# Performance work log

Hardware: AMD Instinct MI355X
Metric: run time of the kernel (lower is better)

## Reference

```python
import jax, jax.numpy as jnp
import numpy as np

IGNORE_ID = -1
NEG_INF = -jnp.inf


def ctc_force_align(log_probs, ctc_label):
    """Viterbi forced alignment, vectorized over batch, scan over time.

    log_probs: [B, T, V] log-softmaxed CTC outputs (blank = 0).
    ctc_label: [B, L] int labels in [1, V).
    Returns align: [B, L] float32, begin frame (1-based, t+1) of each label.
    Assumes uniform lengths: input_len = T, target_len = L for every item
    (how the inputs are generated here).
    """
    B, T, V = log_probs.shape
    L = ctc_label.shape[1]
    N = 2 * L + 1  # CTC state lattice: blank,label,blank,...

    labels = jnp.zeros((B, N), dtype=ctc_label.dtype).at[:, 1::2].set(ctc_label)
    # per-state emission log-prob: [B, T, N]
    lab_b = jnp.broadcast_to(labels[:, None, :], (B, T, N))
    lp_states = jnp.take_along_axis(log_probs, lab_b, axis=2)

    idx = jnp.arange(N)
    ihalf = idx.astype(jnp.float32) / 2.0
    # labels[i] == labels[i-2] (False for i < 2)
    same_label = labels == jnp.concatenate(
        [jnp.full((B, 2), -1, labels.dtype), labels[:, :-2]], axis=1)
    two_way = (idx % 2 == 0)[None, :] | (idx == 1)[None, :] | same_label  # [B, N]

    ts = jnp.arange(T).astype(jnp.float32)
    # infeasible if i/2 > t or L - i/2 > T - t  (float division as in original)
    feas = ~((ihalf[None, :] > ts[:, None]) |
             (float(L) - ihalf[None, :] > float(T) - ts[:, None]))  # [T, N]

    a0 = jnp.where(idx[None, :] < 2, lp_states[:, 0, :], NEG_INF)  # [B, N]

    def shift(x, k):
        return jnp.pad(x, ((0, 0), (k, 0)), constant_values=NEG_INF)[:, :N]

    def step(a_prev, inputs):
        lp_t, feas_t = inputs  # [B, N], [N]
        p0, p1, p2 = a_prev, shift(a_prev, 1), shift(a_prev, 2)
        val_two = jnp.where(p0 > p1, idx, idx - 1)
        best0 = (p0 > p1) & (p0 > p2)
        best1 = (p1 > p0) & (p1 > p2)
        val_three = jnp.where(best0, idx, jnp.where(best1, idx - 1, idx - 2))
        val = jnp.where(idx[None, :] == 0, 0,
                        jnp.where(two_way, val_two, val_three))
        off = idx[None, :] - val
        a_sel = jnp.where(off == 0, p0, jnp.where(off == 1, p1, p2))
        a_new = jnp.where(feas_t[None, :], a_sel + lp_t, NEG_INF)
        v = jnp.where(feas_t[None, :], val, 0).astype(jnp.int32)
        return a_new, v

    lp_tb = jnp.moveaxis(lp_states, 1, 0)  # [T, B, N]
    a_final, v_all = jax.lax.scan(step, a0, (lp_tb[1:], feas[1:]))
    # v_all: [T-1, B, N] for t = 1 .. T-1
    v_all = jnp.moveaxis(v_all, 1, 0)  # [B, T-1, N]

    def backtrace(a_fin, v_seq):  # a_fin: [N], v_seq: [T-1, N]
        use_last = a_fin[N - 1] > a_fin[N - 2]
        pre0 = jnp.where(use_last, N - 1, N - 2)
        align0 = jnp.where((jnp.arange(L) == L - 1) & (~use_last),
                           float(T), 0.0).astype(jnp.float32)
        tp1 = jnp.arange(T - 1, 0, -1)  # t+1 values: T-1 .. 1
        lidx = jnp.arange(L)

        def bstep(carry, inp):
            pre, align = carry
            v_row, t1 = inp
            pre = v_row[pre]
            odd = (pre % 2) == 1
            align = jnp.where((lidx == pre // 2) & odd,
                              t1.astype(jnp.float32), align)
            return (pre, align), None

        (_, align), _ = jax.lax.scan(bstep, (pre0, align0), (v_seq[::-1], tp1))
        return align

    return jax.vmap(backtrace)(a_final, v_all)  # [B, L]


def setup_inputs() -> dict:
    key = jax.random.key(0)
    k0, k1, k2, k3, k4 = jax.random.split(key, 5)
    B, layers, L, T, V = 16, 6, 200, 1000, 5000
    ali_out = jax.random.uniform(k0, (B, layers, L + 1, T), dtype=jnp.float32)
    ali_beg = jax.random.randint(k1, (B, L), 0, T, dtype=jnp.int32)
    ali_end = jax.random.randint(k2, (B, L), 0, T, dtype=jnp.int32)
    enc_mask = jnp.zeros((B, T), dtype=bool)
    ctc_out = jax.random.normal(k3, (B, T, V), dtype=jnp.float32)
    ctc_label = jax.random.randint(k4, (B, L), 1, V, dtype=jnp.int32)
    ctc_len = jnp.full((B,), T, dtype=jnp.int32)
    return {"ali_out": ali_out, "ali_beg": ali_beg, "ali_end": ali_end,
            "enc_mask": enc_mask, "ctc_out": ctc_out,
            "ctc_label": ctc_label, "ctc_len": ctc_len}


def reference(ali_out, ali_beg, ali_end, enc_mask, ctc_out, ctc_label, ctc_len):
    B, layers, olen, ilen = ali_out.shape
    hlen = enc_mask.shape[1]  # == ilen == T
    # forced alignment on detached (stop-gradient) log-probs
    log_probs = jax.lax.stop_gradient(jax.nn.log_softmax(ctc_out, axis=2))
    ali = ctc_force_align(log_probs, ctc_label)  # [B, L] float32
    # expected position: matmul with pos_vec = [1..hlen], drop last output step
    pos = jnp.arange(1, hlen + 1, dtype=ali_out.dtype)
    ali_pos = jnp.einsum('bloi,i->blo', ali_out, pos)[:, :, :-1]  # [B, layers, L]
    ylens = jnp.sum(ali_beg != IGNORE_ID, axis=1)  # [B]
    mask = jnp.arange(olen - 1)[None, :] >= ylens[:, None]  # [B, L] pad mask
    total = (~mask).sum().astype(ali_out.dtype) * layers
    lat = jnp.where(mask[:, None, :], 0.0, ali_pos - ali[:, None, :])
    return (lat ** 2).sum() / total / hlen
```

## Files before the change

### kernel.cpp

```cpp
#include <hip/hip_runtime.h>
#include <hip/hip_bf16.h>
#include <math.h>

#define NEGINF (-INFINITY)

typedef float f32x4 __attribute__((ext_vector_type(4)));

__device__ __forceinline__ float wave_max_f(float m) {
#pragma unroll
  for (int d = 32; d > 0; d >>= 1) m = fmaxf(m, __shfl_xor(m, d, 64));
  return m;
}
__device__ __forceinline__ float wave_sum_f(float s) {
#pragma unroll
  for (int d = 32; d > 0; d >>= 1) s += __shfl_xor(s, d, 64);
  return s;
}
__device__ __forceinline__ int wave_sum_i(int s) {
#pragma unroll
  for (int d = 32; d > 0; d >>= 1) s += __shfl_xor(s, d, 64);
  return s;
}

__device__ __forceinline__ float dpp_wave_shr1(float x) {
  int r = __builtin_amdgcn_mov_dpp(__float_as_int(x), 0x138, 0xf, 0xf, true);
  return __int_as_float(r);
}

__global__ __launch_bounds__(256) void kA_lse_gather(
    const float* __restrict__ ctc_out, const int* __restrict__ ctc_label,
    float* __restrict__ lp, int B, int T, int V, int L, int LANES,
    int TPAD, int ROWF)
{
  extern __shared__ float shrow[];
  __shared__ float wred[4];
  int row = blockIdx.x;
  int b = row / T;
  int t = row - b * T;
  int tid = threadIdx.x;
  int w = tid >> 6;
  const float* x = ctc_out + (size_t)row * V;

  float m = NEGINF;
  int nf4 = V >> 2;
  for (int k = tid; k < nf4; k += 256) {
    float4 v = reinterpret_cast<const float4*>(x)[k];
    reinterpret_cast<float4*>(shrow)[k] = v;
    m = fmaxf(m, fmaxf(fmaxf(v.x, v.y), fmaxf(v.z, v.w)));
  }
  for (int k = (nf4 << 2) + tid; k < V; k += 256) {
    float v = x[k]; shrow[k] = v; m = fmaxf(m, v);
  }
  m = wave_max_f(m);
  if ((tid & 63) == 0) wred[w] = m;
  __syncthreads();
  float bm = fmaxf(fmaxf(wred[0], wred[1]), fmaxf(wred[2], wred[3]));
  __syncthreads();

  float s = 0.f;
  for (int k = tid; k < V; k += 256) s += __expf(shrow[k] - bm);
  s = wave_sum_f(s);
  if ((tid & 63) == 0) wred[w] = s;
  __syncthreads();
  float lse = bm + __logf(wred[0] + wred[1] + wred[2] + wred[3]);

  const int* lab = ctc_label + (size_t)b * L;
  float* dst = lp + ((size_t)b * TPAD + t) * ROWF;
  int nq = LANES * 4;
  for (int idx = tid; idx < nq; idx += 256) {
    int sl = idx >> 2, q = idx & 3;
    int jb = ((7 * sl) >> 1) + 1;
    int j = jb + q; if (j > L) j = L;
    int vi = lab[j - 1];
    if ((unsigned)vi >= (unsigned)V) vi = 0;
    dst[idx] = shrow[vi] - lse;
  }
  if (tid == 0) dst[nq] = shrow[0] - lse;
}

__global__ __launch_bounds__(64, 1) void kB_viterbi(
    const float* __restrict__ lp, const int* __restrict__ ctc_label,
    float* __restrict__ ali, int B, int T, int L, int TPAD, int ROWF)
{
  extern __shared__ float smemf[];
  const int N = 2 * L + 1;
  const int LANES = (N + 6) / 7;
  const unsigned STGB = (unsigned)(16 * ROWF * 4);
  const unsigned OFFROW = 2u * STGB;

  int b = blockIdx.x;
  int lane = threadIdx.x;
  const float* lpb = lp + (size_t)b * TPAD * ROWF;
  const int* lab = ctc_label + (size_t)b * L;
  int qlane = (lane < LANES) ? lane : (LANES - 1);
  int blkoff = LANES * 4;
  unsigned sbase = __builtin_amdgcn_groupstaticsize();

  int i0 = lane * 7;
  float a0v, a1v, a2v, a3v, a4v, a5v, a6v;
  int twv[7];
  int tlo[7];
  unsigned rng[7];
#pragma unroll
  for (int s = 0; s < 7; ++s) {
    int i = i0 + s;
    bool valid = (i < N);
    bool odd = (i & 1) != 0;
    int li = (i - 1) >> 1;
    int myl = (odd && valid) ? lab[li] : 0;
    int pl  = (odd && valid && i >= 3) ? lab[li - 1] : -1;
    twv[s] = ((!odd) || (i == 1) || (myl == pl)) ? 1 : 0;
    if (valid) {
      tlo[s] = (i + 1) >> 1;
      int thi = T - L + (i >> 1);
      rng[s] = (unsigned)(thi - tlo[s]);
    } else {
      tlo[s] = T + 2;
      rng[s] = 0u;
    }
  }

  {
    f32x4 q00 = reinterpret_cast<const f32x4*>(lpb)[qlane];
    float bl00 = lpb[blkoff];
    a0v = (i0 == 0) ? bl00 : NEGINF;
    a1v = NEGINF; a2v = NEGINF; a3v = NEGINF; a4v = NEGINF; a5v = NEGINF;
    a6v = NEGINF;
    if (i0 + 1 == 1) a1v = q00.x;
  }

  int ndma = ROWF >> 4;
#define DMA_SEG(row0, bufidx)                                                 \
  {                                                                           \
    const float* gsrc_ = lpb + (size_t)(row0) * ROWF;                         \
    char* dbase_ = (char*)smemf + (unsigned)(bufidx) * STGB;                  \
    for (int kk_ = 0; kk_ < ndma; ++kk_) {                                    \
      __builtin_amdgcn_global_load_lds(                                       \
          (const unsigned int*)(gsrc_ + (size_t)kk_ * 256 + lane * 4),        \
          (unsigned int*)(dbase_ + kk_ * 1024), 16, 0, 0);                    \
    }                                                                         \
  }

  f32x4 rqA, rqB, rqC, rqD;
  float rblA, rblB, rblC, rblD;

#define RINGRD(SL, qaddr, baddr)                                              \
  asm volatile("ds_read_b128 %0, %1" : "=v"(rq##SL) : "v"(qaddr));            \
  asm volatile("ds_read_b32 %0, %1" : "=v"(rbl##SL) : "v"(baddr));

#define STEP_F(s, P0, P1, P2, OCS, ND, OD)                                    \
  {                                                                           \
    bool c01 = (P0) > (P1);                                                   \
    float m01 = c01 ? (P0) : (P1);                                            \
    bool take3 = (twv[s] == 0) && !(m01 > (P2));                              \
    float asel = take3 ? (P2) : m01;                                          \
    OD = take3 ? 2u : (c01 ? 0u : 1u);                                        \
    float lps = (((lane + (s)) & 1) ? (OCS) : blc);                           \
    ND = asel + lps;                                                          \
  }

#define STEP_S(s, P0, P1, P2, OCS, ND, OD)                                    \
  {                                                                           \
    STEP_F(s, P0, P1, P2, OCS, ND, OD)                                        \
    bool feas = (unsigned)(tt - tlo[s]) <= rng[s];                            \
    ND = feas ? ND : NEGINF;                                                  \
  }

#define BODY(SL, UL, STEPM)                                                   \
  {                                                                           \
    const int tt = tt0 + (UL);                                                \
    asm volatile("s_waitcnt lgkmcnt(9)");                                     \
    __builtin_amdgcn_sched_barrier(0);                                        \
    float blc = rbl##SL;                                                      \
    f32x4 oc = rq##SL;                                                        \
    float n0, n1, n2, n3, n4, n5, n6;                                         \
    unsigned o0, o1, o2, o3, o4, o5, o6;                                      \
    STEPM(5, a5v, a4v, a3v, oc.z, n5, o5)                                     \
    STEPM(6, a6v, a5v, a4v, oc.w, n6, o6)                                     \
    float t6n = dpp_wave_shr1(n6);                                            \
    float t5n = dpp_wave_shr1(n5);                                            \
    STEPM(0, a0v, t6, t5, oc.x, n0, o0)                                       \
    STEPM(1, a1v, a0v, t6, oc.x, n1, o1)                                      \
    STEPM(2, a2v, a1v, a0v, oc.y, n2, o2)                                     \
    STEPM(3, a3v, a2v, a1v, oc.y, n3, o3)                                     \
    STEPM(4, a4v, a3v, a2v, oc.z, n4, o4)                                     \
    unsigned pack = o0 | (o1 << 2) | (o2 << 4) | (o3 << 6) | (o4 << 8) |      \
                    (o5 << 10) | (o6 << 12);                                  \
    asm volatile("ds_write_b16 %0, %1" :: "v"(wa), "v"(pack));                \
    wa += 128;                                                                \
    if ((UL) == 12) {                                                         \
      asm volatile("s_waitcnt vmcnt(0)" ::: "memory");                        \
      __builtin_amdgcn_sched_barrier(0);                                      \
    }                                                                         \
    {                                                                         \
      unsigned qa = ((UL) < 12) ? (qcur + ((UL) + 4) * 960u)                  \
                                : (qnxt + ((UL) - 12) * 960u);                \
      unsigned ba = ((UL) < 12) ? (bcur + ((UL) + 4) * 960u)                  \
                                : (bnxt + ((UL) - 12) * 960u);                \
      RINGRD(SL, qa, ba)                                                      \
    }                                                                         \
    a0v = n0; a1v = n1; a2v = n2; a3v = n3; a4v = n4; a5v = n5; a6v = n6;     \
    t6 = (lane == 0) ? NEGINF : t6n;                                          \
    t5 = (lane == 0) ? NEGINF : t5n;                                          \
  }

  DMA_SEG(1, 0)
  asm volatile("s_waitcnt vmcnt(0)" ::: "memory");
  __builtin_amdgcn_sched_barrier(0);

  unsigned wa = sbase + OFFROW + (unsigned)(lane * 2);
  {
    unsigned q0 = sbase + (unsigned)(qlane * 16);
    unsigned b0 = sbase + (unsigned)(blkoff * 4);
    RINGRD(A, q0 + 0u * 960u, b0 + 0u * 960u)
    RINGRD(B, q0 + 1u * 960u, b0 + 1u * 960u)
    RINGRD(C, q0 + 2u * 960u, b0 + 2u * 960u)
    RINGRD(D, q0 + 3u * 960u, b0 + 3u * 960u)
    unsigned zz = 0;
    asm volatile("ds_write_b16 %0, %1" :: "v"(wa), "v"(zz));
    asm volatile("ds_write_b16 %0, %1" :: "v"(wa), "v"(zz));
    asm volatile("ds_write_b16 %0, %1" :: "v"(wa), "v"(zz));
  }

  float t6 = __shfl_up(a6v, 1, 64);
  float t5 = __shfl_up(a5v, 1, 64);
  if (lane == 0) { t6 = NEGINF; t5 = NEGINF; }

  int NSEG = (T - 1 + 15) >> 4;
  for (int sg = 0; sg < NSEG; ++sg) {
    int tt0 = 1 + 16 * sg;
    unsigned bufc = sbase + (unsigned)(sg & 1) * STGB;
    unsigned bufn = sbase + (unsigned)((sg + 1) & 1) * STGB;
    unsigned qcur = bufc + (unsigned)(qlane * 16);
    unsigned qnxt = bufn + (unsigned)(qlane * 16);
    unsigned bcur = bufc + (unsigned)(blkoff * 4);
    unsigned bnxt = bufn + (unsigned)(blkoff * 4);
    if (sg + 1 < NSEG) { DMA_SEG(tt0 + 16, ((sg + 1) & 1)) }
    int rem = T - tt0;
    bool fast = (rem >= 16) && (tt0 >= L) && (tt0 + 15 <= T - L);
    if (fast) {
      BODY(A, 0, STEP_F)  BODY(B, 1, STEP_F)  BODY(C, 2, STEP_F)
      BODY(D, 3, STEP_F)  BODY(A, 4, STEP_F)  BODY(B, 5, STEP_F)
      BODY(C, 6, STEP_F)  BODY(D, 7, STEP_F)  BODY(A, 8, STEP_F)
      BODY(B, 9, STEP_F)  BODY(C, 10, STEP_F) BODY(D, 11, STEP_F)
      BODY(A, 12, STEP_F) BODY(B, 13, STEP_F) BODY(C, 14, STEP_F)
      BODY(D, 15, STEP_F)
    } else {
      if (0 < rem)  { BODY(A, 0, STEP_S) }
      if (1 < rem)  { BODY(B, 1, STEP_S) }
      if (2 < rem)  { BODY(C, 2, STEP_S) }
      if (3 < rem)  { BODY(D, 3, STEP_S) }
      if (4 < rem)  { BODY(A, 4, STEP_S) }
      if (5 < rem)  { BODY(B, 5, STEP_S) }
      if (6 < rem)  { BODY(C, 6, STEP_S) }
      if (7 < rem)  { BODY(D, 7, STEP_S) }
      if (8 < rem)  { BODY(A, 8, STEP_S) }
      if (9 < rem)  { BODY(B, 9, STEP_S) }
      if (10 < rem) { BODY(C, 10, STEP_S) }
      if (11 < rem) { BODY(D, 11, STEP_S) }
      if (12 < rem) { BODY(A, 12, STEP_S) }
      if (13 < rem) { BODY(B, 13, STEP_S) }
      if (14 < rem) { BODY(C, 14, STEP_S) }
      if (15 < rem) { BODY(D, 15, STEP_S) }
    }
  }
#undef BODY
#undef STEP_S
#undef STEP_F
#undef RINGRD
#undef DMA_SEG

  asm volatile("s_waitcnt vmcnt(0) lgkmcnt(0)" ::: "memory");
  __builtin_amdgcn_sched_barrier(0);

  int iN1 = N - 1, iN2 = N - 2;
  auto pick = [&](int sIdx) {
    float r = a0v;
    r = (sIdx == 1) ? a1v : r;
    r = (sIdx == 2) ? a2v : r;
    r = (sIdx == 3) ? a3v : r;
    r = (sIdx == 4) ? a4v : r;
    r = (sIdx == 5) ? a5v : r;
    r = (sIdx == 6) ? a6v : r;
    return r;
  };
  float vlast = __shfl(pick(iN1 % 7), iN1 / 7, 64);
  float vprev = __shfl(pick(iN2 % 7), iN2 / 7, 64);
  bool use_last = vlast > vprev;
  int pre = use_last ? iN1 : iN2;

  float al[4] = {0.f, 0.f, 0.f, 0.f};
  {
    int lbl = L - 1; int rr = lbl >> 6, ln = lbl & 63;
#pragma unroll
    for (int r = 0; r < 4; ++r)
      if (!use_last && rr == r && lane == ln) al[r] = (float)T;
  }

  const unsigned short* offrow =
      (const unsigned short*)((char*)smemf + OFFROW);
  int t = T - 1;
  int g = pre / 7, mm = pre - g * 7;
  while (t >= 1) {
    int K = (t < 7) ? t : 7;
    int pcur = g * 7 + mm;
    int gmax = g;
    unsigned short w0v = offrow[(size_t)(t - 1) * 64 + g];
    unsigned short cw[7][3];
    int gmn[7];
#pragma unroll
    for (int j = 1; j < 7; ++j) {
      if (j < K) {
        int lo = pcur - 2 * j; if (lo < 0) lo = 0;
        int gm = lo / 7;
        gmn[j] = gm;
#pragma unroll
        for (int r = 0; r < 3; ++r) {
          int gg = gm + r; if (gg > gmax) gg = gmax;
          cw[j][r] = offrow[(size_t)(t - 1 - j) * 64 + gg];
        }
      }
    }
#pragma unroll
    for (int j = 0; j < 7; ++j) {
      if (j < K) {
        unsigned w;
        if (j == 0) {
          w = w0v;
        } else {
          int gi = g - gmn[j];
          unsigned wva = cw[j][0], wvb = cw[j][1], wvc = cw[j][2];
          w = (gi == 0) ? wva : ((gi == 1) ? wvb : wvc);
        }
        unsigned off = (w >> (2 * mm)) & 3u;
        mm -= (int)off;
        bool bor = mm < 0;
        g = bor ? (g - 1) : g;
        mm = bor ? (mm + 7) : mm;
        int cur = g * 7 + mm;
        if (cur & 1) {
          int lbl = cur >> 1;
          int rr = lbl >> 6, ln = lbl & 63;
#pragma unroll
          for (int r = 0; r < 4; ++r)
            if (rr == r && lane == ln) al[r] = (float)(t - j);
        }
      }
    }
    t -= K;
  }

#pragma unroll
  for (int r = 0; r < 4; ++r) {
    int l = lane + 64 * r;
    if (l < L) ali[(size_t)b * L + l] = al[r];
  }
}

__global__ __launch_bounds__(256) void kC_rows(
    const float* __restrict__ ali_out, const float* __restrict__ ali,
    const int* __restrict__ ali_beg, float* __restrict__ partials,
    int B, int layers, int L, int T)
{
  __shared__ float ps[4];
  int wid = threadIdx.x >> 6, lane = threadIdx.x & 63;
  int row = blockIdx.x * 4 + wid;
  int nrows = B * layers * L;
  float val = 0.f;
  if (row < nrows) {
    int o = row % L;
    int bl = row / L;
    int layer = bl % layers;
    int b = bl / layers;
    const float* x = ali_out + ((size_t)(b * layers + layer) * (L + 1) + o) * T;
    float s = 0.f;
    if ((T & 3) == 0) {
      int nf4 = T >> 2;
      for (int k = lane; k < nf4; k += 64) {
        float4 v = reinterpret_cast<const float4*>(x)[k];
        float base = (float)(4 * k);
        s += v.x * (base + 1.f) + v.y * (base + 2.f) +
             v.z * (base + 3.f) + v.w * (base + 4.f);
      }
    } else {
      for (int k = lane; k < T; k += 64) s += x[k] * (float)(k + 1);
    }
    s = wave_sum_f(s);
    int cnt = 0;
    for (int l = lane; l < L; l += 64)
      cnt += (ali_beg[(size_t)b * L + l] != -1) ? 1 : 0;
    cnt = wave_sum_i(cnt);
    if (lane == 0) {
      float lat = (o >= cnt) ? 0.f : (s - ali[(size_t)b * L + o]);
      val = lat * lat;
    }
  }
  if (lane == 0) ps[wid] = val;
  __syncthreads();
  if (threadIdx.x == 0) partials[blockIdx.x] = ps[0] + ps[1] + ps[2] + ps[3];
}

__global__ __launch_bounds__(256) void kD_final(
    const float* __restrict__ partials, int nparts,
    const int* __restrict__ ali_beg, int BL, int layers, int T,
    float* __restrict__ out)
{
  __shared__ float wred[4];
  __shared__ int wcnt[4];
  int tid = threadIdx.x, w = tid >> 6;
  float s = 0.f;
  for (int k = tid; k < nparts; k += 256) s += partials[k];
  s = wave_sum_f(s);
  int c = 0;
  for (int k = tid; k < BL; k += 256) c += (ali_beg[k] != -1) ? 1 : 0;
  c = wave_sum_i(c);
  if ((tid & 63) == 0) { wred[w] = s; wcnt[w] = c; }
  __syncthreads();
  if (tid == 0) {
    float ss = wred[0] + wred[1] + wred[2] + wred[3];
    float total = (float)(wcnt[0] + wcnt[1] + wcnt[2] + wcnt[3]) * (float)layers;
    out[0] = ss / total / (float)T;
  }
}

extern "C" void kernel_launch(void* const* d_in, const int* in_sizes, int n_in,
                              void* d_out, int out_size, void* d_ws, size_t ws_size,
                              hipStream_t stream)
{
  const float* ali_out   = (const float*)d_in[0];
  const int*   ali_beg   = (const int*)d_in[1];
  const float* ctc_out   = (const float*)d_in[4];
  const int*   ctc_label = (const int*)d_in[5];

  int B = in_sizes[6];
  int L = in_sizes[1] / B;
  int T = in_sizes[3] / B;
  int V = (int)((long long)in_sizes[4] / ((long long)B * T));
  int layers = (int)((long long)in_sizes[0] / ((long long)B * (L + 1) * T));

  int N = 2 * L + 1;
  int LANES = (N + 6) / 7;
  int ROWF = LANES * 4 + 8;
  int TPAD = T + 64;

  float* lp = (float*)d_ws;
  float* ali = lp + (size_t)B * TPAD * ROWF;
  float* partials = ali + (size_t)B * L;
  int nrows = B * layers * L;
  int gridC = (nrows + 3) / 4;

  size_t shA = (size_t)V * sizeof(float);
  hipLaunchKernelGGL(kA_lse_gather, dim3(B * T), dim3(256), shA, stream,
                     ctc_out, ctc_label, lp, B, T, V, L, LANES, TPAD, ROWF);

  size_t shB = (size_t)2 * 16 * ROWF * sizeof(float) + (size_t)(T - 1) * 128;
  hipFuncSetAttribute(reinterpret_cast<const void*>(kB_viterbi),
                      hipFuncAttributeMaxDynamicSharedMemorySize, (int)shB);
  hipLaunchKernelGGL(kB_viterbi, dim3(B), dim3(64), shB, stream,
                     lp, ctc_label, ali, B, T, L, TPAD, ROWF);

  hipLaunchKernelGGL(kC_rows, dim3(gridC), dim3(256), 0, stream,
                     ali_out, ali, ali_beg, partials, B, layers, L, T);

  hipLaunchKernelGGL(kD_final, dim3(1), dim3(256), 0, stream,
                     partials, gridC, ali_beg, B * L, layers, T, (float*)d_out);
}
```

Baseline: 498.9 us.

## Deepen LDS read ring to eight slots and restructure DMA/wait schedule

Expands the register ring of prefetched LDS reads from four to eight slots, so each step's emission data is requested eight steps ahead. The next segment's global-to-LDS DMA now starts inside the first step of each segment, with full waits at steps 0 and 8 in place of a per-step lgkmcnt(9) wait. The feasibility-free fast path is removed, so every full segment applies the feasibility mask. The trade-off is more VGPRs, extra feasibility work on every step, and coarser full-drain waits that may stall the serial recurrence.

```diff
diff --git a/kernel.cpp b/kernel.cpp
--- a/kernel.cpp
+++ b/kernel.cpp
@@ -139,16 +139,17 @@
           (const unsigned int*)(gsrc_ + (size_t)kk_ * 256 + lane * 4),        \
           (unsigned int*)(dbase_ + kk_ * 1024), 16, 0, 0);                    \
     }                                                                         \
-  }
-
-  f32x4 rqA, rqB, rqC, rqD;
-  float rblA, rblB, rblC, rblD;
+    __builtin_amdgcn_sched_barrier(0);                                        \
+  }
+
+  f32x4 rqA, rqB, rqC, rqD, rqE, rqF, rqG, rqH;
+  float rblA, rblB, rblC, rblD, rblE, rblF, rblG, rblH;
 
 #define RINGRD(SL, qaddr, baddr)                                              \
   asm volatile("ds_read_b128 %0, %1" : "=v"(rq##SL) : "v"(qaddr));            \
   asm volatile("ds_read_b32 %0, %1" : "=v"(rbl##SL) : "v"(baddr));
 
-#define STEP_F(s, P0, P1, P2, OCS, ND, OD)                                    \
+#define STEP(s, P0, P1, P2, OCS, ND, OD)                                      \
   {                                                                           \
     bool c01 = (P0) > (P1);                                                   \
     float m01 = c01 ? (P0) : (P1);                                            \
@@ -157,46 +158,78 @@
     OD = take3 ? 2u : (c01 ? 0u : 1u);                                        \
     float lps = (((lane + (s)) & 1) ? (OCS) : blc);                           \
     ND = asel + lps;                                                          \
-  }
-
-#define STEP_S(s, P0, P1, P2, OCS, ND, OD)                                    \
-  {                                                                           \
-    STEP_F(s, P0, P1, P2, OCS, ND, OD)                                        \
     bool feas = (unsigned)(tt - tlo[s]) <= rng[s];                            \
     ND = feas ? ND : NEGINF;                                                  \
   }
 
-#define BODY(SL, UL, STEPM)                                                   \
+#define BODY(SL, UL)                                                          \
   {                                                                           \
     const int tt = tt0 + (UL);                                                \
-    asm volatile("s_waitcnt lgkmcnt(9)");                                     \
+    if ((UL) == 0) {                                                          \
+      asm volatile("s_waitcnt lgkmcnt(0)");                                   \
+      __builtin_amdgcn_sched_barrier(0);                                      \
+      if (sg + 1 < NSEG) { DMA_SEG(tt0 + 16, ((sg + 1) & 1)) }                \
+    }                                                                         \
+    if ((UL) == 8) {                                                          \
+      asm volatile("s_waitcnt vmcnt(0) lgkmcnt(0)");                          \
+      __builtin_amdgcn_sched_barrier(0);                                      \
+    }                                                                         \
+    float blc = rbl##SL;                                                      \
+    f32x4 oc = rq##SL;                                                        \
+    float n0, n1, n2, n3, n4, n5, n6;                                         \
+    unsigned o0, o1, o2, o3, o4, o5, o6;                                      \
+    STEP(5, a5v, a4v, a3v, oc.z, n5, o5)                                      \
+    STEP(6, a6v, a5v, a4v, oc.w, n6, o6)                                      \
+    float t6n = dpp_wave_shr1(n6);                                            \
+    float t5n = dpp_wave_shr1(n5);                                            \
+    STEP(0, a0v, t6, t5, oc.x, n0, o0)                                        \
+    STEP(1, a1v, a0v, t6, oc.x, n1, o1)                                       \
+    STEP(2, a2v, a1v, a0v, oc.y, n2, o2)                                      \
+    STEP(3, a3v, a2v, a1v, oc.y, n3, o3)                                      \
+    STEP(4, a4v, a3v, a2v, oc.z, n4, o4)                                      \
+    unsigned pack = o0 | (o1 << 2) | (o2 << 4) | (o3 << 6) | (o4 << 8) |      \
+                    (o5 << 10) | (o6 << 12);                                  \
+    asm volatile("ds_write_b16 %0, %1" :: "v"(wa), "v"(pack));                \
+    wa += 128;                                                                \
+    {                                                                         \
+      unsigned qa = ((UL) < 8) ? (qcur + ((UL) + 8) * 960u)                   \
+                               : (qnxt + ((UL) - 8) * 960u);                  \
+      unsigned ba = ((UL) < 8) ? (bcur + ((UL) + 8) * 960u)                   \
+                               : (bnxt + ((UL) - 8) * 960u);                  \
+      RINGRD(SL, qa, ba)                                                      \
+    }                                                                         \
+    a0v = n0; a1v = n1; a2v = n2; a3v = n3; a4v = n4; a5v = n5; a6v = n6;     \
+    t6 = (lane == 0) ? NEGINF : t6n;                                          \
+    t5 = (lane == 0) ? NEGINF : t5n;                                          \
+  }
+
+#define TBODY(SL, UL)                                                         \
+  {                                                                           \
+    const int tt = tt0 + (UL);                                                \
+    asm volatile("s_waitcnt vmcnt(0) lgkmcnt(0)");                            \
     __builtin_amdgcn_sched_barrier(0);                                        \
     float blc = rbl##SL;                                                      \
     f32x4 oc = rq##SL;                                                        \
     float n0, n1, n2, n3, n4, n5, n6;                                         \
     unsigned o0, o1, o2, o3, o4, o5, o6;                                      \
-    STEPM(5, a5v, a4v, a3v, oc.z, n5, o5)                                     \
-    STEPM(6, a6v, a5v, a4v, oc.w, n6, o6)                                     \
+    STEP(5, a5v, a4v, a3v, oc.z, n5, o5)                                      \
+    STEP(6, a6v, a5v, a4v, oc.w, n6, o6)                                      \
     float t6n = dpp_wave_shr1(n6);                                            \
     float t5n = dpp_wave_shr1(n5);                                            \
-    STEPM(0, a0v, t6, t5, oc.x, n0, o0)                                       \
-    STEPM(1, a1v, a0v, t6, oc.x, n1, o1)                                      \
-    STEPM(2, a2v, a1v, a0v, oc.y, n2, o2)                                     \
-    STEPM(3, a3v, a2v, a1v, oc.y, n3, o3)                                     \
-    STEPM(4, a4v, a3v, a2v, oc.z, n4, o4)                                     \
+    STEP(0, a0v, t6, t5, oc.x, n0, o0)                                        \
+    STEP(1, a1v, a0v, t6, oc.x, n1, o1)                                       \
+    STEP(2, a2v, a1v, a0v, oc.y, n2, o2)                                      \
+    STEP(3, a3v, a2v, a1v, oc.y, n3, o3)                                      \
+    STEP(4, a4v, a3v, a2v, oc.z, n4, o4)                                      \
     unsigned pack = o0 | (o1 << 2) | (o2 << 4) | (o3 << 6) | (o4 << 8) |      \
                     (o5 << 10) | (o6 << 12);                                  \
     asm volatile("ds_write_b16 %0, %1" :: "v"(wa), "v"(pack));                \
     wa += 128;                                                                \
-    if ((UL) == 12) {                                                         \
-      asm volatile("s_waitcnt vmcnt(0)" ::: "memory");                        \
-      __builtin_amdgcn_sched_barrier(0);                                      \
-    }                                                                         \
     {                                                                         \
-      unsigned qa = ((UL) < 12) ? (qcur + ((UL) + 4) * 960u)                  \
-                                : (qnxt + ((UL) - 12) * 960u);                \
-      unsigned ba = ((UL) < 12) ? (bcur + ((UL) + 4) * 960u)                  \
-                                : (bnxt + ((UL) - 12) * 960u);                \
+      unsigned qa = ((UL) < 8) ? (qcur + ((UL) + 8) * 960u)                   \
+                               : (qnxt + ((UL) - 8) * 960u);                  \
+      unsigned ba = ((UL) < 8) ? (bcur + ((UL) + 8) * 960u)                   \
+                               : (bnxt + ((UL) - 8) * 960u);                  \
       RINGRD(SL, qa, ba)                                                      \
     }                                                                         \
     a0v = n0; a1v = n1; a2v = n2; a3v = n3; a4v = n4; a5v = n5; a6v = n6;     \
@@ -205,7 +238,7 @@
   }
 
   DMA_SEG(1, 0)
-  asm volatile("s_waitcnt vmcnt(0)" ::: "memory");
+  asm volatile("s_waitcnt vmcnt(0) lgkmcnt(0)");
   __builtin_amdgcn_sched_barrier(0);
 
   unsigned wa = sbase + OFFROW + (unsigned)(lane * 2);
@@ -216,10 +249,10 @@
     RINGRD(B, q0 + 1u * 960u, b0 + 1u * 960u)
     RINGRD(C, q0 + 2u * 960u, b0 + 2u * 960u)
     RINGRD(D, q0 + 3u * 960u, b0 + 3u * 960u)
-    unsigned zz = 0;
-    asm volatile("ds_write_b16 %0, %1" :: "v"(wa), "v"(zz));
-    asm volatile("ds_write_b16 %0, %1" :: "v"(wa), "v"(zz));
-    asm volatile("ds_write_b16 %0, %1" :: "v"(wa), "v"(zz));
+    RINGRD(E, q0 + 4u * 960u, b0 + 4u * 960u)
+    RINGRD(F, q0 + 5u * 960u, b0 + 5u * 960u)
+    RINGRD(G, q0 + 6u * 960u, b0 + 6u * 960u)
+    RINGRD(H, q0 + 7u * 960u, b0 + 7u * 960u)
   }
 
   float t6 = __shfl_up(a6v, 1, 64);
@@ -235,38 +268,34 @@
     unsigned qnxt = bufn + (unsigned)(qlane * 16);
     unsigned bcur = bufc + (unsigned)(blkoff * 4);
     unsigned bnxt = bufn + (unsigned)(blkoff * 4);
-    if (sg + 1 < NSEG) { DMA_SEG(tt0 + 16, ((sg + 1) & 1)) }
     int rem = T - tt0;
-    bool fast = (rem >= 16) && (tt0 >= L) && (tt0 + 15 <= T - L);
-    if (fast) {
-      BODY(A, 0, STEP_F)  BODY(B, 1, STEP_F)  BODY(C, 2, STEP_F)
-      BODY(D, 3, STEP_F)  BODY(A, 4, STEP_F)  BODY(B, 5, STEP_F)
-      BODY(C, 6, STEP_F)  BODY(D, 7, STEP_F)  BODY(A, 8, STEP_F)
-      BODY(B, 9, STEP_F)  BODY(C, 10, STEP_F) BODY(D, 11, STEP_F)
-      BODY(A, 12, STEP_F) BODY(B, 13, STEP_F) BODY(C, 14, STEP_F)
-      BODY(D, 15, STEP_F)
+    if (rem >= 16) {
+      BODY(A, 0)  BODY(B, 1)  BODY(C, 2)  BODY(D, 3)
+      BODY(E, 4)  BODY(F, 5)  BODY(G, 6)  BODY(H, 7)
+      BODY(A, 8)  BODY(B, 9)  BODY(C, 10) BODY(D, 11)
+      BODY(E, 12) BODY(F, 13) BODY(G, 14) BODY(H, 15)
     } else {
-      if (0 < rem)  { BODY(A, 0, STEP_S) }
-      if (1 < rem)  { BODY(B, 1, STEP_S) }
-      if (2 < rem)  { BODY(C, 2, STEP_S) }
-      if (3 < rem)  { BODY(D, 3, STEP_S) }
-      if (4 < rem)  { BODY(A, 4, STEP_S) }
-      if (5 < rem)  { BODY(B, 5, STEP_S) }
-      if (6 < rem)  { BODY(C, 6, STEP_S) }
-      if (7 < rem)  { BODY(D, 7, STEP_S) }
-      if (8 < rem)  { BODY(A, 8, STEP_S) }
-      if (9 < rem)  { BODY(B, 9, STEP_S) }
-      if (10 < rem) { BODY(C, 10, STEP_S) }
-      if (11 < rem) { BODY(D, 11, STEP_S) }
-      if (12 < rem) { BODY(A, 12, STEP_S) }
-      if (13 < rem) { BODY(B, 13, STEP_S) }
-      if (14 < rem) { BODY(C, 14, STEP_S) }
-      if (15 < rem) { BODY(D, 15, STEP_S) }
-    }
-  }
+      if (0 < rem)  { TBODY(A, 0) }
+      if (1 < rem)  { TBODY(B, 1) }
+      if (2 < rem)  { TBODY(C, 2) }
+      if (3 < rem)  { TBODY(D, 3) }
+      if (4 < rem)  { TBODY(E, 4) }
+      if (5 < rem)  { TBODY(F, 5) }
+      if (6 < rem)  { TBODY(G, 6) }
+      if (7 < rem)  { TBODY(H, 7) }
+      if (8 < rem)  { TBODY(A, 8) }
+      if (9 < rem)  { TBODY(B, 9) }
+      if (10 < rem) { TBODY(C, 10) }
+      if (11 < rem) { TBODY(D, 11) }
+      if (12 < rem) { TBODY(E, 12) }
+      if (13 < rem) { TBODY(F, 13) }
+      if (14 < rem) { TBODY(G, 14) }
+      if (15 < rem) { TBODY(H, 15) }
+    }
+  }
+#undef TBODY
 #undef BODY
-#undef STEP_S
-#undef STEP_F
+#undef STEP
 #undef RINGRD
 #undef DMA_SEG
 
```

Measured after the change: 523.9 us. 5.0% more time.

## Replace LDS DMA ring with direct 8-deep register-prefetched global loads in Viterbi

Applied to the files above, without the earlier changes.

The Viterbi kernel stops staging emission rows through a double-buffered LDS ring filled by global_load_lds. Each lane now issues global_load_dwordx4 straight into an 8-entry register ring, and the blank emission is taken via readlane from lane 58 instead of a separate LDS read. The intent is to take the LDS round-trip and the per-segment DMA waits off the serial time recurrence and to shrink shared memory to just the backpointer table. In exchange, global load latency is exposed within an 8-step prefetch window. The padding columns are zeroed in kA so the extra lane can read defined data.

```diff
diff --git a/kernel.cpp b/kernel.cpp
--- a/kernel.cpp
+++ b/kernel.cpp
@@ -76,6 +76,7 @@
     dst[idx] = shrow[vi] - lse;
   }
   if (tid == 0) dst[nq] = shrow[0] - lse;
+  for (int z = nq + 1 + tid; z < ROWF; z += 256) dst[z] = 0.f;
 }
 
 __global__ __launch_bounds__(64, 1) void kB_viterbi(
@@ -85,16 +86,14 @@
   extern __shared__ float smemf[];
   const int N = 2 * L + 1;
   const int LANES = (N + 6) / 7;
-  const unsigned STGB = (unsigned)(16 * ROWF * 4);
-  const unsigned OFFROW = 2u * STGB;
 
   int b = blockIdx.x;
   int lane = threadIdx.x;
   const float* lpb = lp + (size_t)b * TPAD * ROWF;
   const int* lab = ctc_label + (size_t)b * L;
-  int qlane = (lane < LANES) ? lane : (LANES - 1);
+  int qlane = (lane < LANES) ? lane : LANES;
+  if (qlane > LANES) qlane = LANES;
   int blkoff = LANES * 4;
-  unsigned sbase = __builtin_amdgcn_groupstaticsize();
 
   int i0 = lane * 7;
   float a0v, a1v, a2v, a3v, a4v, a5v, a6v;
@@ -121,7 +120,7 @@
   }
 
   {
-    f32x4 q00 = reinterpret_cast<const f32x4*>(lpb)[qlane];
+    f32x4 q00 = *reinterpret_cast<const f32x4*>(lpb + qlane * 4);
     float bl00 = lpb[blkoff];
     a0v = (i0 == 0) ? bl00 : NEGINF;
     a1v = NEGINF; a2v = NEGINF; a3v = NEGINF; a4v = NEGINF; a5v = NEGINF;
@@ -129,24 +128,21 @@
     if (i0 + 1 == 1) a1v = q00.x;
   }
 
-  int ndma = ROWF >> 4;
-#define DMA_SEG(row0, bufidx)                                                 \
-  {                                                                           \
-    const float* gsrc_ = lpb + (size_t)(row0) * ROWF;                         \
-    char* dbase_ = (char*)smemf + (unsigned)(bufidx) * STGB;                  \
-    for (int kk_ = 0; kk_ < ndma; ++kk_) {                                    \
-      __builtin_amdgcn_global_load_lds(                                       \
-          (const unsigned int*)(gsrc_ + (size_t)kk_ * 256 + lane * 4),        \
-          (unsigned int*)(dbase_ + kk_ * 1024), 16, 0, 0);                    \
-    }                                                                         \
-  }
-
-  f32x4 rqA, rqB, rqC, rqD;
-  float rblA, rblB, rblC, rblD;
-
-#define RINGRD(SL, qaddr, baddr)                                              \
-  asm volatile("ds_read_b128 %0, %1" : "=v"(rq##SL) : "v"(qaddr));            \
-  asm volatile("ds_read_b32 %0, %1" : "=v"(rbl##SL) : "v"(baddr));
+  f32x4 rq0, rq1, rq2, rq3, rq4, rq5, rq6, rq7;
+  unsigned short* offrow_w = (unsigned short*)smemf;
+
+  asm volatile("s_waitcnt vmcnt(0) lgkmcnt(0)");
+  __builtin_amdgcn_sched_barrier(0);
+
+  unsigned long long base64 = (unsigned long long)lpb;
+  unsigned voff = (unsigned)(qlane * 16) + 960u;
+
+#define LOADQ(SL)                                                             \
+  asm volatile("global_load_dwordx4 %0, %1, %2"                               \
+               : "=v"(rq##SL) : "v"(voff), "s"(base64));                      \
+  voff += 960u;
+
+  LOADQ(1) LOADQ(2) LOADQ(3) LOADQ(4) LOADQ(5) LOADQ(6) LOADQ(7) LOADQ(0)
 
 #define STEP_F(s, P0, P1, P2, OCS, ND, OD)                                    \
   {                                                                           \
@@ -166,112 +162,68 @@
     ND = feas ? ND : NEGINF;                                                  \
   }
 
-#define BODY(SL, UL, STEPM)                                                   \
+#define BODYC(SL, K, STEPM)                                                   \
   {                                                                           \
-    const int tt = tt0 + (UL);                                                \
-    asm volatile("s_waitcnt lgkmcnt(9)");                                     \
+    const int tt = tt0 + (K);                                                 \
+    asm volatile("s_waitcnt vmcnt(7)");                                       \
     __builtin_amdgcn_sched_barrier(0);                                        \
-    float blc = rbl##SL;                                                      \
-    f32x4 oc = rq##SL;                                                        \
+    float blc = __int_as_float(                                               \
+        __builtin_amdgcn_readlane(__float_as_int(rq##SL.x), 58));             \
     float n0, n1, n2, n3, n4, n5, n6;                                         \
     unsigned o0, o1, o2, o3, o4, o5, o6;                                      \
-    STEPM(5, a5v, a4v, a3v, oc.z, n5, o5)                                     \
-    STEPM(6, a6v, a5v, a4v, oc.w, n6, o6)                                     \
+    STEPM(5, a5v, a4v, a3v, rq##SL.z, n5, o5)                                 \
+    STEPM(6, a6v, a5v, a4v, rq##SL.w, n6, o6)                                 \
     float t6n = dpp_wave_shr1(n6);                                            \
     float t5n = dpp_wave_shr1(n5);                                            \
-    STEPM(0, a0v, t6, t5, oc.x, n0, o0)                                       \
-    STEPM(1, a1v, a0v, t6, oc.x, n1, o1)                                      \
-    STEPM(2, a2v, a1v, a0v, oc.y, n2, o2)                                     \
-    STEPM(3, a3v, a2v, a1v, oc.y, n3, o3)                                     \
-    STEPM(4, a4v, a3v, a2v, oc.z, n4, o4)                                     \
+    STEPM(0, a0v, t6, t5, rq##SL.x, n0, o0)                                   \
+    STEPM(1, a1v, a0v, t6, rq##SL.x, n1, o1)                                  \
+    STEPM(2, a2v, a1v, a0v, rq##SL.y, n2, o2)                                 \
+    STEPM(3, a3v, a2v, a1v, rq##SL.y, n3, o3)                                 \
+    STEPM(4, a4v, a3v, a2v, rq##SL.z, n4, o4)                                 \
     unsigned pack = o0 | (o1 << 2) | (o2 << 4) | (o3 << 6) | (o4 << 8) |      \
                     (o5 << 10) | (o6 << 12);                                  \
-    asm volatile("ds_write_b16 %0, %1" :: "v"(wa), "v"(pack));                \
-    wa += 128;                                                                \
-    if ((UL) == 12) {                                                         \
-      asm volatile("s_waitcnt vmcnt(0)" ::: "memory");                        \
-      __builtin_amdgcn_sched_barrier(0);                                      \
-    }                                                                         \
-    {                                                                         \
-      unsigned qa = ((UL) < 12) ? (qcur + ((UL) + 4) * 960u)                  \
-                                : (qnxt + ((UL) - 12) * 960u);                \
-      unsigned ba = ((UL) < 12) ? (bcur + ((UL) + 4) * 960u)                  \
-                                : (bnxt + ((UL) - 12) * 960u);                \
-      RINGRD(SL, qa, ba)                                                      \
-    }                                                                         \
+    offrow_w[(size_t)(tt - 1) * 64 + lane] = (unsigned short)pack;            \
+    LOADQ(SL)                                                                 \
     a0v = n0; a1v = n1; a2v = n2; a3v = n3; a4v = n4; a5v = n5; a6v = n6;     \
     t6 = (lane == 0) ? NEGINF : t6n;                                          \
     t5 = (lane == 0) ? NEGINF : t5n;                                          \
   }
 
-  DMA_SEG(1, 0)
-  asm volatile("s_waitcnt vmcnt(0)" ::: "memory");
-  __builtin_amdgcn_sched_barrier(0);
-
-  unsigned wa = sbase + OFFROW + (unsigned)(lane * 2);
-  {
-    unsigned q0 = sbase + (unsigned)(qlane * 16);
-    unsigned b0 = sbase + (unsigned)(blkoff * 4);
-    RINGRD(A, q0 + 0u * 960u, b0 + 0u * 960u)
-    RINGRD(B, q0 + 1u * 960u, b0 + 1u * 960u)
-    RINGRD(C, q0 + 2u * 960u, b0 + 2u * 960u)
-    RINGRD(D, q0 + 3u * 960u, b0 + 3u * 960u)
-    unsigned zz = 0;
-    asm volatile("ds_write_b16 %0, %1" :: "v"(wa), "v"(zz));
-    asm volatile("ds_write_b16 %0, %1" :: "v"(wa), "v"(zz));
-    asm volatile("ds_write_b16 %0, %1" :: "v"(wa), "v"(zz));
-  }
-
   float t6 = __shfl_up(a6v, 1, 64);
   float t5 = __shfl_up(a5v, 1, 64);
   if (lane == 0) { t6 = NEGINF; t5 = NEGINF; }
 
-  int NSEG = (T - 1 + 15) >> 4;
-  for (int sg = 0; sg < NSEG; ++sg) {
-    int tt0 = 1 + 16 * sg;
-    unsigned bufc = sbase + (unsigned)(sg & 1) * STGB;
-    unsigned bufn = sbase + (unsigned)((sg + 1) & 1) * STGB;
-    unsigned qcur = bufc + (unsigned)(qlane * 16);
-    unsigned qnxt = bufn + (unsigned)(qlane * 16);
-    unsigned bcur = bufc + (unsigned)(blkoff * 4);
-    unsigned bnxt = bufn + (unsigned)(blkoff * 4);
-    if (sg + 1 < NSEG) { DMA_SEG(tt0 + 16, ((sg + 1) & 1)) }
+  int tt0 = 1;
+  for (; tt0 + 8 <= T; tt0 += 8) {
+    if (tt0 >= L && tt0 + 7 <= T - L) {
+      BODYC(1, 0, STEP_F) BODYC(2, 1, STEP_F) BODYC(3, 2, STEP_F)
+      BODYC(4, 3, STEP_F) BODYC(5, 4, STEP_F) BODYC(6, 5, STEP_F)
+      BODYC(7, 6, STEP_F) BODYC(0, 7, STEP_F)
+    } else {
+      BODYC(1, 0, STEP_S) BODYC(2, 1, STEP_S) BODYC(3, 2, STEP_S)
+      BODYC(4, 3, STEP_S) BODYC(5, 4, STEP_S) BODYC(6, 5, STEP_S)
+      BODYC(7, 6, STEP_S) BODYC(0, 7, STEP_S)
+    }
+  }
+  {
     int rem = T - tt0;
-    bool fast = (rem >= 16) && (tt0 >= L) && (tt0 + 15 <= T - L);
-    if (fast) {
-      BODY(A, 0, STEP_F)  BODY(B, 1, STEP_F)  BODY(C, 2, STEP_F)
-      BODY(D, 3, STEP_F)  BODY(A, 4, STEP_F)  BODY(B, 5, STEP_F)
-      BODY(C, 6, STEP_F)  BODY(D, 7, STEP_F)  BODY(A, 8, STEP_F)
-      BODY(B, 9, STEP_F)  BODY(C, 10, STEP_F) BODY(D, 11, STEP_F)
-      BODY(A, 12, STEP_F) BODY(B, 13, STEP_F) BODY(C, 14, STEP_F)
-      BODY(D, 15, STEP_F)
-    } else {
-      if (0 < rem)  { BODY(A, 0, STEP_S) }
-      if (1 < rem)  { BODY(B, 1, STEP_S) }
-      if (2 < rem)  { BODY(C, 2, STEP_S) }
-      if (3 < rem)  { BODY(D, 3, STEP_S) }
-      if (4 < rem)  { BODY(A, 4, STEP_S) }
-      if (5 < rem)  { BODY(B, 5, STEP_S) }
-      if (6 < rem)  { BODY(C, 6, STEP_S) }
-      if (7 < rem)  { BODY(D, 7, STEP_S) }
-      if (8 < rem)  { BODY(A, 8, STEP_S) }
-      if (9 < rem)  { BODY(B, 9, STEP_S) }
-      if (10 < rem) { BODY(C, 10, STEP_S) }
-      if (11 < rem) { BODY(D, 11, STEP_S) }
-      if (12 < rem) { BODY(A, 12, STEP_S) }
-      if (13 < rem) { BODY(B, 13, STEP_S) }
-      if (14 < rem) { BODY(C, 14, STEP_S) }
-      if (15 < rem) { BODY(D, 15, STEP_S) }
-    }
-  }
-#undef BODY
+    if (rem > 0) { BODYC(1, 0, STEP_S) }
+    if (rem > 1) { BODYC(2, 1, STEP_S) }
+    if (rem > 2) { BODYC(3, 2, STEP_S) }
+    if (rem > 3) { BODYC(4, 3, STEP_S) }
+    if (rem > 4) { BODYC(5, 4, STEP_S) }
+    if (rem > 5) { BODYC(6, 5, STEP_S) }
+    if (rem > 6) { BODYC(7, 6, STEP_S) }
+  }
+#undef BODYC
 #undef STEP_S
 #undef STEP_F
-#undef RINGRD
-#undef DMA_SEG
+#undef LOADQ
 
   asm volatile("s_waitcnt vmcnt(0) lgkmcnt(0)" ::: "memory");
   __builtin_amdgcn_sched_barrier(0);
+  asm volatile("" :: "v"(rq0), "v"(rq1), "v"(rq2), "v"(rq3));
+  asm volatile("" :: "v"(rq4), "v"(rq5), "v"(rq6), "v"(rq7));
 
   int iN1 = N - 1, iN2 = N - 2;
   auto pick = [&](int sIdx) {
@@ -297,8 +249,7 @@
       if (!use_last && rr == r && lane == ln) al[r] = (float)T;
   }
 
-  const unsigned short* offrow =
-      (const unsigned short*)((char*)smemf + OFFROW);
+  const unsigned short* offrow = (const unsigned short*)smemf;
   int t = T - 1;
   int g = pre / 7, mm = pre - g * 7;
   while (t >= 1) {
@@ -453,7 +404,7 @@
   hipLaunchKernelGGL(kA_lse_gather, dim3(B * T), dim3(256), shA, stream,
                      ctc_out, ctc_label, lp, B, T, V, L, LANES, TPAD, ROWF);
 
-  size_t shB = (size_t)2 * 16 * ROWF * sizeof(float) + (size_t)(T - 1) * 128;
+  size_t shB = (size_t)(T - 1) * 128;
   hipFuncSetAttribute(reinterpret_cast<const void*>(kB_viterbi),
                       hipFuncAttributeMaxDynamicSharedMemorySize, (int)shB);
   hipLaunchKernelGGL(kB_viterbi, dim3(B), dim3(64), shB, stream,
```

After: 462.7 us. 1.08x faster.
